# Kernel tuning notes

Measured on AMD Instinct MI355X. Metric: run time of the kernel, lower is better.

The kernel has to match this reference:

```python
import jax, jax.numpy as jnp
import numpy as np

NUM_HEADS = 16
NUM_KV_HEADS = 4
HEAD_DIM = 80
EMBED_DIM = 1280
EPS = 1e-6
NEG_INF = -1e30


def rms_norm(x, w):
    # per-head RMSNorm over last dim, computed in fp32 like the torch module
    xf = x.astype(jnp.float32)
    var = jnp.mean(xf * xf, axis=-1, keepdims=True)
    return (w * (xf * jax.lax.rsqrt(var + EPS))).astype(x.dtype)


def rotate_half(x):
    x1, x2 = jnp.split(x, 2, axis=-1)
    return jnp.concatenate([-x2, x1], axis=-1)


def apply_rope(x, freqs):
    # x: [T, H, hd], freqs: [T, hd]
    cos = jnp.cos(freqs)[:, None, :].astype(jnp.float32)
    sin = jnp.sin(freqs)[:, None, :].astype(jnp.float32)
    xf = x.astype(jnp.float32)
    return (xf * cos + rotate_half(xf) * sin).astype(x.dtype)


def setup_inputs() -> dict:
    key = jax.random.key(0)
    ks = jax.random.split(key, 6)
    T = 4096
    n_seqs = 8  # 8 packed vision sequences of 512 tokens each
    hidden_states = jax.random.normal(ks[0], (T, EMBED_DIM), dtype=jnp.float32)
    cu_seqlens = jnp.arange(n_seqs + 1, dtype=jnp.int32) * (T // n_seqs)
    rotary_pos_emb = jax.random.normal(ks[1], (T, HEAD_DIM), dtype=jnp.float32)
    qkv_rows = (NUM_HEADS + 2 * NUM_KV_HEADS) * HEAD_DIM  # 1920
    w_qkv = jax.random.normal(ks[2], (qkv_rows, EMBED_DIM), dtype=jnp.float32) * (EMBED_DIM ** -0.5)
    w_o = jax.random.normal(ks[3], (EMBED_DIM, NUM_HEADS * HEAD_DIM), dtype=jnp.float32) * ((NUM_HEADS * HEAD_DIM) ** -0.5)
    q_norm_w = jnp.ones((HEAD_DIM,), dtype=jnp.float32)
    k_norm_w = jnp.ones((HEAD_DIM,), dtype=jnp.float32)
    return {
        'hidden_states': hidden_states,
        'cu_seqlens': cu_seqlens,
        'rotary_pos_emb': rotary_pos_emb,
        'w_qkv': w_qkv,
        'w_o': w_o,
        'q_norm_w': q_norm_w,
        'k_norm_w': k_norm_w,
    }


def reference(hidden_states, cu_seqlens, rotary_pos_emb, w_qkv, w_o, q_norm_w, k_norm_w):
    T = hidden_states.shape[0]
    H, KV, hd = NUM_HEADS, NUM_KV_HEADS, HEAD_DIM

    qkv = hidden_states @ w_qkv.T  # [T, (H+2KV)*hd]
    q, k, v = jnp.split(qkv, [H * hd, (H + KV) * hd], axis=-1)
    q = q.reshape(T, H, hd)
    k = k.reshape(T, KV, hd)
    v = v.reshape(T, KV, hd)

    q = rms_norm(q, q_norm_w)
    k = rms_norm(k, k_norm_w)
    q = apply_rope(q, rotary_pos_emb)
    k = apply_rope(k, rotary_pos_emb)

    # GQA: repeat_interleave kv heads to match query heads
    rep = H // KV
    k = jnp.repeat(k, rep, axis=1)  # [T, H, hd]
    v = jnp.repeat(v, rep, axis=1)

    # block-diagonal varlen mask from cu_seqlens
    seg = jnp.searchsorted(cu_seqlens[1:], jnp.arange(T, dtype=cu_seqlens.dtype), side='right')
    mask = seg[:, None] == seg[None, :]  # [T, T]

    scale = hd ** -0.5
    scores = jnp.einsum('thd,shd->hts', q, k) * scale  # [H, T, T]
    scores = jnp.where(mask[None, :, :], scores, NEG_INF)
    probs = jax.nn.softmax(scores, axis=-1)
    attn = jnp.einsum('hts,shd->thd', probs, v)  # [T, H, hd]

    out = attn.reshape(T, H * hd) @ w_o.T  # [T, EMBED_DIM]
    return out
```

## Files before the change

kernel.cpp:

```cpp
#include <hip/hip_runtime.h>
#include <hip/hip_bf16.h>

#define H_Q 16
#define H_KV 4
#define HD 80
#define QKV_ROW 1920
#define K_OFF 1280
#define EMB 1280
#define QT 128
#define KC 64
#define KROW 80
#define VTS 4096

typedef unsigned short u16;
typedef unsigned int u32;
typedef __attribute__((ext_vector_type(8))) short bf16x8;
typedef __attribute__((ext_vector_type(4))) float f32x4;

__device__ inline u16 f2bf(float f) {
  unsigned u = __float_as_uint(f);
  unsigned r = (u + 0x7FFFu + ((u >> 16) & 1u)) >> 16;
  return (u16)r;
}
__device__ inline float bf2f(u16 v) { return __uint_as_float(((unsigned)v) << 16); }

__device__ inline void cvt4(const float* __restrict__ in, u16* __restrict__ out, int q) {
  float4 v = *reinterpret_cast<const float4*>(in + q * 4);
  ushort4 o;
  o.x = f2bf(v.x); o.y = f2bf(v.y); o.z = f2bf(v.z); o.w = f2bf(v.w);
  *reinterpret_cast<ushort4*>(out + q * 4) = o;
}

__global__ __launch_bounds__(256) void prep_kernel(const float* __restrict__ hidden,
                                                   const float* __restrict__ w_qkv,
                                                   const float* __restrict__ w_o,
                                                   const int* __restrict__ cu, int n_seq, int T,
                                                   u16* __restrict__ hid_bf,
                                                   u16* __restrict__ wqkv_bf,
                                                   u16* __restrict__ wo_bf,
                                                   int* __restrict__ seg,
                                                   int nq_hid, int nq_wqkv, int nq_wo) {
  const int i = blockIdx.x * 256 + threadIdx.x;
  if (i < T) {
    int s = 0;
    for (int k = 1; k <= n_seq; ++k) s += (i >= cu[k]) ? 1 : 0;
    seg[i] = s;
  }
  int q = i;
  if (q < nq_hid) { cvt4(hidden, hid_bf, q); return; }
  q -= nq_hid;
  if (q < nq_wqkv) { cvt4(w_qkv, wqkv_bf, q); return; }
  q -= nq_wqkv;
  if (q < nq_wo) cvt4(w_o, wo_bf, q);
}

template <typename OUT, bool VSPLIT>
__global__ __launch_bounds__(256) void gemm_bf16(const u16* __restrict__ A,
                                                 const u16* __restrict__ B,
                                                 OUT* __restrict__ C,
                                                 u16* __restrict__ vt,
                                                 int M, int N, int K, int ldc,
                                                 int gx, int nwg) {
  __shared__ u16 As[3][128 * 32];
  __shared__ u16 Bs[3][64 * 32];
  const int tid = threadIdx.x;
  const int id = blockIdx.x;
  const int sw = (id & 7) * (nwg >> 3) + (id >> 3);
  const int bm = (sw / gx) * 128;
  const int bn = (sw % gx) * 64;
  const int w = tid >> 6;
  const int l = tid & 63;
  const int wr = (w >> 1) * 64, wc = (w & 1) * 32;
  const int fr = l & 15;
  const int fq = l >> 4;
  const int arow = tid >> 2, acol = (tid & 3) * 8;

  f32x4 acc[4][2];
  #pragma unroll
  for (int mi = 0; mi < 4; ++mi)
    #pragma unroll
    for (int ni = 0; ni < 2; ++ni) acc[mi][ni] = (f32x4){0.f, 0.f, 0.f, 0.f};

  #define GSTAGE(buf, k0)                                                             \
    do {                                                                              \
      _Pragma("unroll")                                                               \
      for (int it = 0; it < 2; ++it) {                                                \
        const u16* ga = A + (size_t)(bm + it * 64 + arow) * K + (k0) + acol;          \
        __builtin_amdgcn_global_load_lds(                                             \
            (const __attribute__((address_space(1))) unsigned int*)ga,                \
            (__attribute__((address_space(3))) unsigned int*)&As[buf][it * 2048 + tid * 8], 16, 0, 0); \
      }                                                                               \
      const u16* gb = B + (size_t)(bn + arow) * K + (k0) + acol;                      \
      __builtin_amdgcn_global_load_lds(                                               \
          (const __attribute__((address_space(1))) unsigned int*)gb,                  \
          (__attribute__((address_space(3))) unsigned int*)&Bs[buf][tid * 8], 16, 0, 0); \
    } while (0)

  const int nt = K >> 5;
  GSTAGE(0, 0);
  GSTAGE(1, 32);

  int cur = 0;
  for (int t = 0; t < nt; ++t) {
    if (t + 2 < nt) {
      const int nb = (cur + 2) % 3;
      GSTAGE(nb, (t + 2) * 32);
      asm volatile("s_waitcnt vmcnt(6)" ::: "memory");
    } else if (t + 1 < nt) {
      asm volatile("s_waitcnt vmcnt(3)" ::: "memory");
    } else {
      asm volatile("s_waitcnt vmcnt(0)" ::: "memory");
    }
    __builtin_amdgcn_s_barrier();
    __builtin_amdgcn_sched_barrier(0);

    bf16x8 af[4], bfr[2];
    #pragma unroll
    for (int mi = 0; mi < 4; ++mi)
      af[mi] = *reinterpret_cast<const bf16x8*>(&As[cur][(wr + mi * 16 + fr) * 32 + fq * 8]);
    #pragma unroll
    for (int ni = 0; ni < 2; ++ni)
      bfr[ni] = *reinterpret_cast<const bf16x8*>(&Bs[cur][(wc + ni * 16 + fr) * 32 + fq * 8]);
    __builtin_amdgcn_s_setprio(1);
    #pragma unroll
    for (int mi = 0; mi < 4; ++mi)
      #pragma unroll
      for (int ni = 0; ni < 2; ++ni)
        acc[mi][ni] = __builtin_amdgcn_mfma_f32_16x16x32_bf16(af[mi], bfr[ni], acc[mi][ni], 0, 0, 0);
    __builtin_amdgcn_s_setprio(0);

    __builtin_amdgcn_sched_barrier(0);
    __builtin_amdgcn_s_barrier();
    cur = (cur + 1) % 3;
  }
  #undef GSTAGE

  #pragma unroll
  for (int mi = 0; mi < 4; ++mi)
    #pragma unroll
    for (int ni = 0; ni < 2; ++ni) {
      const int col = bn + wc + ni * 16 + fr;
      const int row0 = bm + wr + mi * 16 + fq * 4;
      if (VSPLIT && col >= 1600) {
        ushort4 o;
        o.x = f2bf(acc[mi][ni][0]); o.y = f2bf(acc[mi][ni][1]);
        o.z = f2bf(acc[mi][ni][2]); o.w = f2bf(acc[mi][ni][3]);
        *reinterpret_cast<ushort4*>(&vt[(size_t)(col - 1600) * VTS + row0]) = o;
      } else {
        #pragma unroll
        for (int j = 0; j < 4; ++j) {
          if constexpr (sizeof(OUT) == 2)
            C[(size_t)(row0 + j) * ldc + col] = f2bf(acc[mi][ni][j]);
          else
            C[(size_t)(row0 + j) * ldc + col] = acc[mi][ni][j];
        }
      }
    }
}

__global__ __launch_bounds__(320) void norm_rope_bf(u16* __restrict__ qkv,
                                                    const float* __restrict__ freqs,
                                                    const float* __restrict__ qw,
                                                    const float* __restrict__ kw) {
  const int t = blockIdx.x;
  const int tid = threadIdx.x;
  __shared__ float cs[HD], sn[HD];
  __shared__ float wq[HD], wk[HD];
  __shared__ float xs[5][HD];
  if (tid < HD) {
    const float f = freqs[(size_t)t * HD + tid];
    cs[tid] = __cosf(f);
    sn[tid] = __sinf(f);
    wq[tid] = qw[tid];
    wk[tid] = kw[tid];
  }
  __syncthreads();
  const int w = tid >> 6, lane = tid & 63;
  #pragma unroll
  for (int i = 0; i < 4; ++i) {
    const int hh = w * 4 + i;
    const bool is_q = (hh < H_Q);
    u16* x = qkv + (size_t)t * QKV_ROW + (is_q ? hh * HD : K_OFF + (hh - H_Q) * HD);
    const float* wt = is_q ? wq : wk;
    float a = bf2f(x[lane]);
    float b = (lane < HD - 64) ? bf2f(x[64 + lane]) : 0.0f;
    float ss = a * a + b * b;
    #pragma unroll
    for (int off = 32; off; off >>= 1) ss += __shfl_down(ss, off);
    ss = __shfl(ss, 0);
    const float inv = rsqrtf(ss * (1.0f / HD) + 1e-6f);
    xs[w][lane] = a * inv * wt[lane];
    if (lane < HD - 64) xs[w][64 + lane] = b * inv * wt[64 + lane];
    __syncthreads();
    {
      const int d = lane;
      const float rot = (d < HD / 2) ? -xs[w][d + HD / 2] : xs[w][d - HD / 2];
      x[d] = f2bf(xs[w][d] * cs[d] + rot * sn[d]);
    }
    if (lane < HD - 64) {
      const int d = 64 + lane;
      const float rot = (d < HD / 2) ? -xs[w][d + HD / 2] : xs[w][d - HD / 2];
      x[d] = f2bf(xs[w][d] * cs[d] + rot * sn[d]);
    }
    __syncthreads();
  }
}

__global__ __launch_bounds__(512) void attn_v7(const u16* __restrict__ qkv,
                                               const u16* __restrict__ vt,
                                               const int* __restrict__ seg,
                                               const int* __restrict__ cu,
                                               int T,
                                               u16* __restrict__ attn_bf) {
  __shared__ u16 K_lds[2][KC * KROW + 16];
  __shared__ u16 V_lds[2][96 * 64];
  __shared__ u32 Pw[8][16 * 36];
  __shared__ int ksegs[2][KC];

  const int t0 = blockIdx.x * QT;
  const int h = blockIdx.y;
  const int kvh = h >> 2;
  const int tid = threadIdx.x;
  const int w = tid >> 6, l = tid & 63;
  const int g = l >> 4, fr = l & 15;

  for (int i = tid; i < 2 * 16 * 32; i += 512) {
    const int b = i >> 9, r = (i >> 5) & 15, c = i & 31;
    ((u32*)V_lds[b])[(80 + r) * 32 + c] = (r == 0) ? 0x3f803f80u : 0u;
  }
  if (tid < 16) { K_lds[0][KC * KROW + tid] = 0; K_lds[1][KC * KROW + tid] = 0; }

  const int s0_ = seg[t0], s1_ = seg[t0 + QT - 1];
  const int kbeg = cu[s0_], kend = cu[s1_ + 1];
  const bool fast = (s0_ == s1_) && (((kend - kbeg) & (KC - 1)) == 0) && ((kbeg & 7) == 0);

  const int qrow = t0 + w * 16 + fr;
  const u16* qp = qkv + (size_t)qrow * QKV_ROW + h * HD;
  bf16x8 qa0 = *reinterpret_cast<const bf16x8*>(qp + g * 8);
  bf16x8 qa1 = *reinterpret_cast<const bf16x8*>(qp + 32 + g * 8);
  bf16x8 qa2 = (g < 2) ? *reinterpret_cast<const bf16x8*>(qp + 64 + g * 8)
                       : (bf16x8)(short)0;
  const int qsgl = seg[qrow];

  f32x4 acc[6];
  #pragma unroll
  for (int dt = 0; dt < 6; ++dt) acc[dt] = (f32x4){0.f, 0.f, 0.f, 0.f};
  const float C2 = 0.16130010464f;

  #define ASTAGE(nb, cc)                                                               \
    do {                                                                               \
      for (int i = tid; i < 640; i += 512) {                                           \
        const int kr = i / 10, kc_ = i - kr * 10;                                      \
        const u16* gk = qkv + (size_t)((cc) + kr) * QKV_ROW + K_OFF + kvh * HD + kc_ * 8; \
        __builtin_amdgcn_global_load_lds(                                              \
            (const __attribute__((address_space(1))) u32*)gk,                          \
            (__attribute__((address_space(3))) u32*)&K_lds[nb][i * 8], 16, 0, 0);      \
        const int vr = i >> 3, vs = i & 7;                                             \
        const u16* gv = vt + (size_t)(kvh * HD + vr) * VTS + (cc) + ((vs ^ (vr & 7)) * 8); \
        __builtin_amdgcn_global_load_lds(                                              \
            (const __attribute__((address_space(1))) u32*)gv,                          \
            (__attribute__((address_space(3))) u32*)&V_lds[nb][i * 8], 16, 0, 0);      \
      }                                                                                \
    } while (0)

  #define SSTAGE(nb, cc)                                                               \
    do {                                                                               \
      for (int i = tid; i < KC * 40; i += 512) {                                       \
        const int r = i / 40, ccc = i - r * 40;                                        \
        u32 v = 0;                                                                     \
        if ((cc) + r < kend)                                                           \
          v = reinterpret_cast<const u32*>(qkv + (size_t)((cc) + r) * QKV_ROW + K_OFF + kvh * HD)[ccc]; \
        ((u32*)K_lds[nb])[i] = v;                                                      \
      }                                                                                \
      for (int i = tid; i < HD * KC; i += 512) {                                       \
        const int vr = i >> 6, k = i & 63;                                             \
        u16 v = 0;                                                                     \
        if ((cc) + k < kend)                                                           \
          v = vt[(size_t)(kvh * HD + vr) * VTS + (cc) + k];                            \
        V_lds[nb][vr * 64 + (((k >> 3) ^ (vr & 7)) * 8) + (k & 7)] = v;                \
      }                                                                                \
      if (tid < KC) ksegs[nb][tid] = ((cc) + tid < kend) ? seg[(cc) + tid] : -1;       \
    } while (0)

  if (fast) ASTAGE(0, kbeg); else SSTAGE(0, kbeg);
  __syncthreads();

  const int c3 = (fr & 3) << 2;
  u32* pw = &Pw[w][0];
  const int sA = 4 * (g >> 1) + 2 * (g & 1);

  int nb = 0;
  for (int c = kbeg; c < kend; c += KC) {
    const int cur = nb;
    nb ^= 1;
    if (c + KC < kend) {
      if (fast) ASTAGE(nb, c + KC); else SSTAGE(nb, c + KC);
    }

    const u16* kb = K_lds[cur];
    f32x4 sacc[4];
    #pragma unroll
    for (int f = 0; f < 4; ++f) {
      const u16* kp = kb + (f * 16 + fr) * KROW;
      bf16x8 b0 = *reinterpret_cast<const bf16x8*>(kp + g * 8);
      bf16x8 b1 = *reinterpret_cast<const bf16x8*>(kp + 32 + g * 8);
      bf16x8 b2 = *reinterpret_cast<const bf16x8*>(kp + 64 + g * 8);
      f32x4 s = (f32x4){0.f, 0.f, 0.f, 0.f};
      s = __builtin_amdgcn_mfma_f32_16x16x32_bf16(b0, qa0, s, 0, 0, 0);
      s = __builtin_amdgcn_mfma_f32_16x16x32_bf16(b1, qa1, s, 0, 0, 0);
      s = __builtin_amdgcn_mfma_f32_16x16x32_bf16(b2, qa2, s, 0, 0, 0);
      sacc[f] = s;
    }

    if (fast) {
      #pragma unroll
      for (int f = 0; f < 4; ++f) {
        const float p0 = __builtin_exp2f(sacc[f][0] * C2);
        const float p1 = __builtin_exp2f(sacc[f][1] * C2);
        const float p2 = __builtin_exp2f(sacc[f][2] * C2);
        const float p3 = __builtin_exp2f(sacc[f][3] * C2);
        u32 lo, hi;
        asm("v_cvt_pk_bf16_f32 %0, %1, %2" : "=v"(lo) : "v"(p0), "v"(p1));
        asm("v_cvt_pk_bf16_f32 %0, %1, %2" : "=v"(hi) : "v"(p2), "v"(p3));
        const int sel = (4 * f + g) ^ c3;
        *reinterpret_cast<uint2*>(&pw[fr * 36 + sel * 2]) = make_uint2(lo, hi);
      }
    } else {
      #pragma unroll
      for (int f = 0; f < 4; ++f) {
        float pj[4];
        #pragma unroll
        for (int j = 0; j < 4; ++j) {
          const int kk = f * 16 + g * 4 + j;
          float e = sacc[f][j] * C2;
          if (qsgl != ksegs[cur][kk]) e = -1e30f;
          pj[j] = __builtin_exp2f(e);
        }
        u32 lo, hi;
        asm("v_cvt_pk_bf16_f32 %0, %1, %2" : "=v"(lo) : "v"(pj[0]), "v"(pj[1]));
        asm("v_cvt_pk_bf16_f32 %0, %1, %2" : "=v"(hi) : "v"(pj[2]), "v"(pj[3]));
        const int sel = (4 * f + g) ^ c3;
        *reinterpret_cast<uint2*>(&pw[fr * 36 + sel * 2]) = make_uint2(lo, hi);
      }
    }
    asm volatile("s_waitcnt lgkmcnt(0)" ::: "memory");
    __builtin_amdgcn_sched_barrier(0);
    bf16x8 pa0 = *reinterpret_cast<const bf16x8*>(&pw[fr * 36 + ((sA ^ c3) * 2)]);
    bf16x8 pa1 = *reinterpret_cast<const bf16x8*>(&pw[fr * 36 + (((8 + sA) ^ c3) * 2)]);

    const u16* vb = V_lds[cur];
    #pragma unroll
    for (int dt = 0; dt < 6; ++dt) {
      const int row = dt * 16 + fr;
      const u16* vp = vb + row * 64;
      bf16x8 vb0 = *reinterpret_cast<const bf16x8*>(vp + ((g ^ (fr & 7)) * 8));
      bf16x8 vb1 = *reinterpret_cast<const bf16x8*>(vp + ((((4 + g)) ^ (fr & 7)) * 8));
      acc[dt] = __builtin_amdgcn_mfma_f32_16x16x32_bf16(pa0, vb0, acc[dt], 0, 0, 0);
      acc[dt] = __builtin_amdgcn_mfma_f32_16x16x32_bf16(pa1, vb1, acc[dt], 0, 0, 0);
    }

    __syncthreads();
  }
  #undef ASTAGE
  #undef SSTAGE

  #pragma unroll
  for (int j = 0; j < 4; ++j) {
    const float lsum = __shfl(acc[5][j], l & 48);
    const float il = (lsum > 0.f) ? 1.0f / lsum : 0.f;
    const int row = t0 + w * 16 + g * 4 + j;
    #pragma unroll
    for (int dt = 0; dt < 5; ++dt)
      attn_bf[(size_t)row * EMB + h * HD + dt * 16 + fr] = f2bf(acc[dt][j] * il);
  }
}

extern "C" void kernel_launch(void* const* d_in, const int* in_sizes, int n_in,
                              void* d_out, int out_size, void* d_ws, size_t ws_size,
                              hipStream_t stream) {
  const float* hidden = (const float*)d_in[0];
  const int*   cu     = (const int*)d_in[1];
  const float* rope   = (const float*)d_in[2];
  const float* w_qkv  = (const float*)d_in[3];
  const float* w_o    = (const float*)d_in[4];
  const float* qw     = (const float*)d_in[5];
  const float* kw     = (const float*)d_in[6];
  float* out = (float*)d_out;

  const int T = in_sizes[0] / EMB;
  const int n_seq = in_sizes[1] - 1;

  u16* qkv_bf  = (u16*)d_ws;
  u16* hid_bf  = qkv_bf + (size_t)T * QKV_ROW;
  u16* attn_bf = hid_bf;
  u16* wqkv_bf = hid_bf + (size_t)T * EMB;
  u16* wo_bf   = wqkv_bf + (size_t)QKV_ROW * EMB;
  u16* v_t     = wo_bf + (size_t)EMB * EMB;
  int* segb    = (int*)(v_t + (size_t)320 * 4096 + 64);

  const int nq_hid = T * EMB / 4, nq_wqkv = QKV_ROW * EMB / 4, nq_wo = EMB * EMB / 4;
  const int nq_tot = nq_hid + nq_wqkv + nq_wo;
  prep_kernel<<<(nq_tot + 255) / 256, 256, 0, stream>>>(
      hidden, w_qkv, w_o, cu, n_seq, T, hid_bf, wqkv_bf, wo_bf, segb,
      nq_hid, nq_wqkv, nq_wo);

  {
    const int gx = QKV_ROW / 64, nwg = gx * (T / 128);
    gemm_bf16<u16, true><<<nwg, 256, 0, stream>>>(hid_bf, wqkv_bf, qkv_bf, v_t,
                                                  T, QKV_ROW, EMB, QKV_ROW, gx, nwg);
  }
  norm_rope_bf<<<T, 320, 0, stream>>>(qkv_bf, rope, qw, kw);
  attn_v7<<<dim3(T / QT, H_Q), 512, 0, stream>>>(qkv_bf, v_t, segb, cu, T, attn_bf);
  {
    const int gx = EMB / 64, nwg = gx * (T / 128);
    gemm_bf16<float, false><<<nwg, 256, 0, stream>>>(attn_bf, wo_bf, out, nullptr,
                                                     T, EMB, EMB, EMB, gx, nwg);
  }
}
```

Measured before the change: 121.3 us.

## Use 64-wide K tiles with XOR-swizzled LDS and double buffering in GEMM

The bf16 GEMM now stages K in chunks of 64 instead of 32, so each barrier pair covers twice as many MFMAs. The pipeline drops from triple buffering to double buffering. Shared-memory columns are XOR-swizzled by row to avoid bank conflicts on the wider rows. The cost is less prefetch depth, since only one tile is in flight while the current one computes, and larger LDS use per block.

```diff
diff --git a/kernel.cpp b/kernel.cpp
--- a/kernel.cpp
+++ b/kernel.cpp
@@ -61,8 +61,8 @@
                                                  u16* __restrict__ vt,
                                                  int M, int N, int K, int ldc,
                                                  int gx, int nwg) {
-  __shared__ u16 As[3][128 * 32];
-  __shared__ u16 Bs[3][64 * 32];
+  __shared__ u16 As[2][128 * 64];
+  __shared__ u16 Bs[2][64 * 64];
   const int tid = threadIdx.x;
   const int id = blockIdx.x;
   const int sw = (id & 7) * (nwg >> 3) + (id >> 3);
@@ -73,7 +73,8 @@
   const int wr = (w >> 1) * 64, wc = (w & 1) * 32;
   const int fr = l & 15;
   const int fq = l >> 4;
-  const int arow = tid >> 2, acol = (tid & 3) * 8;
+  const int srow = tid >> 3;
+  const int scol = ((tid & 7) ^ ((tid >> 3) & 7)) * 8;
 
   f32x4 acc[4][2];
   #pragma unroll
@@ -84,54 +85,63 @@
   #define GSTAGE(buf, k0)                                                             \
     do {                                                                              \
       _Pragma("unroll")                                                               \
-      for (int it = 0; it < 2; ++it) {                                                \
-        const u16* ga = A + (size_t)(bm + it * 64 + arow) * K + (k0) + acol;          \
+      for (int it = 0; it < 4; ++it) {                                                \
+        const u16* ga = A + (size_t)(bm + it * 32 + srow) * K + (k0) + scol;          \
         __builtin_amdgcn_global_load_lds(                                             \
             (const __attribute__((address_space(1))) unsigned int*)ga,                \
             (__attribute__((address_space(3))) unsigned int*)&As[buf][it * 2048 + tid * 8], 16, 0, 0); \
       }                                                                               \
-      const u16* gb = B + (size_t)(bn + arow) * K + (k0) + acol;                      \
-      __builtin_amdgcn_global_load_lds(                                               \
-          (const __attribute__((address_space(1))) unsigned int*)gb,                  \
-          (__attribute__((address_space(3))) unsigned int*)&Bs[buf][tid * 8], 16, 0, 0); \
+      _Pragma("unroll")                                                               \
+      for (int it = 0; it < 2; ++it) {                                                \
+        const u16* gb = B + (size_t)(bn + it * 32 + srow) * K + (k0) + scol;          \
+        __builtin_amdgcn_global_load_lds(                                             \
+            (const __attribute__((address_space(1))) unsigned int*)gb,                \
+            (__attribute__((address_space(3))) unsigned int*)&Bs[buf][it * 2048 + tid * 8], 16, 0, 0); \
+      }                                                                               \
     } while (0)
 
-  const int nt = K >> 5;
+  const int nt = K >> 6;
   GSTAGE(0, 0);
-  GSTAGE(1, 32);
-
-  int cur = 0;
+
   for (int t = 0; t < nt; ++t) {
-    if (t + 2 < nt) {
-      const int nb = (cur + 2) % 3;
-      GSTAGE(nb, (t + 2) * 32);
+    const int cur = t & 1;
+    if (t + 1 < nt) {
+      GSTAGE(cur ^ 1, (t + 1) * 64);
       asm volatile("s_waitcnt vmcnt(6)" ::: "memory");
-    } else if (t + 1 < nt) {
-      asm volatile("s_waitcnt vmcnt(3)" ::: "memory");
     } else {
       asm volatile("s_waitcnt vmcnt(0)" ::: "memory");
     }
     __builtin_amdgcn_s_barrier();
     __builtin_amdgcn_sched_barrier(0);
 
-    bf16x8 af[4], bfr[2];
-    #pragma unroll
-    for (int mi = 0; mi < 4; ++mi)
-      af[mi] = *reinterpret_cast<const bf16x8*>(&As[cur][(wr + mi * 16 + fr) * 32 + fq * 8]);
-    #pragma unroll
-    for (int ni = 0; ni < 2; ++ni)
-      bfr[ni] = *reinterpret_cast<const bf16x8*>(&Bs[cur][(wc + ni * 16 + fr) * 32 + fq * 8]);
-    __builtin_amdgcn_s_setprio(1);
+    bf16x8 af[4][2], bfr[2][2];
     #pragma unroll
     for (int mi = 0; mi < 4; ++mi)
       #pragma unroll
-      for (int ni = 0; ni < 2; ++ni)
-        acc[mi][ni] = __builtin_amdgcn_mfma_f32_16x16x32_bf16(af[mi], bfr[ni], acc[mi][ni], 0, 0, 0);
+      for (int kk = 0; kk < 2; ++kk) {
+        const int ps = ((kk * 4 + fq) ^ (fr & 7)) * 8;
+        af[mi][kk] = *reinterpret_cast<const bf16x8*>(&As[cur][(wr + mi * 16 + fr) * 64 + ps]);
+      }
+    #pragma unroll
+    for (int ni = 0; ni < 2; ++ni)
+      #pragma unroll
+      for (int kk = 0; kk < 2; ++kk) {
+        const int ps = ((kk * 4 + fq) ^ (fr & 7)) * 8;
+        bfr[ni][kk] = *reinterpret_cast<const bf16x8*>(&Bs[cur][(wc + ni * 16 + fr) * 64 + ps]);
+      }
+    __builtin_amdgcn_s_setprio(1);
+    #pragma unroll
+    for (int kk = 0; kk < 2; ++kk)
+      #pragma unroll
+      for (int mi = 0; mi < 4; ++mi)
+        #pragma unroll
+        for (int ni = 0; ni < 2; ++ni)
+          acc[mi][ni] = __builtin_amdgcn_mfma_f32_16x16x32_bf16(af[mi][kk], bfr[ni][kk],
+                                                               acc[mi][ni], 0, 0, 0);
     __builtin_amdgcn_s_setprio(0);
 
     __builtin_amdgcn_sched_barrier(0);
     __builtin_amdgcn_s_barrier();
-    cur = (cur + 1) % 3;
   }
   #undef GSTAGE
 
```

After: 115.1 us. 1.05x faster.
